# Optimization experiments

Measured on AMD Instinct MI355X. Metric: run time of the kernel, lower is better.

The kernel has to match this reference:

```python
import jax, jax.numpy as jnp
import numpy as np

D_MODEL = 1024
EXPAND = 2
D_INNER = D_MODEL * EXPAND  # 2048
D_STATE = 16
D_CONV = 4
B, T = 4, 2048


def setup_inputs() -> dict:
    key = jax.random.key(0)
    ks = jax.random.split(key, 8)
    s = 0.02  # small init std for numeric stability
    return {
        "x": jax.random.normal(ks[0], (B, T, D_MODEL), jnp.float32),
        "in_proj_w": jax.random.normal(ks[1], (2 * D_INNER, D_MODEL), jnp.float32) * s,
        "conv_w": jax.random.normal(ks[2], (D_INNER, 1, D_CONV), jnp.float32) * s,
        "conv_b": jnp.zeros((D_INNER,), jnp.float32),
        "x_proj_w": jax.random.normal(ks[3], (2 * D_STATE, D_INNER), jnp.float32) * s,
        "dt_proj_w": jax.random.normal(ks[4], (D_INNER, D_STATE), jnp.float32) * s,
        "dt_proj_b": jnp.zeros((D_INNER,), jnp.float32),
        "D_param": jnp.ones((D_INNER,), jnp.float32),
        "out_proj_w": jax.random.normal(ks[5], (D_MODEL, D_INNER), jnp.float32) * s,
    }


def reference(x, in_proj_w, conv_w, conv_b, x_proj_w, dt_proj_w, dt_proj_b, D_param, out_proj_w):
    Bsz, Tlen, _ = x.shape
    # in_proj (no bias), torch Linear: x @ W.T
    xz = jnp.einsum('btd,ed->bte', x, in_proj_w)            # [B,T,2*D_INNER]
    x_inner, z = jnp.split(xz, 2, axis=-1)                   # each [B,T,D_INNER]
    # depthwise causal conv1d: left-pad d_conv-1, take first T outputs
    xc = jnp.transpose(x_inner, (0, 2, 1))                   # [B,D_INNER,T]
    xc = jax.lax.conv_general_dilated(
        xc, conv_w, window_strides=(1,), padding=[(D_CONV - 1, 0)],
        feature_group_count=D_INNER)
    xc = xc + conv_b[None, :, None]
    x_conv = jax.nn.silu(jnp.transpose(xc, (0, 2, 1)))       # [B,T,D_INNER]
    # x_proj -> (B_ssm, C_ssm); C_ssm is unused by the simplified scan (faithful)
    x_ssm = jnp.einsum('btd,ed->bte', x_conv, x_proj_w)      # [B,T,2*D_STATE]
    B_ssm, C_ssm = jnp.split(x_ssm, 2, axis=-1)
    dt = jax.nn.softplus(jnp.einsum('btn,dn->btd', B_ssm, dt_proj_w) + dt_proj_b)  # [B,T,D_INNER]
    # simplified selective scan: EMA with scalar-per-timestep gate
    alpha = jax.nn.sigmoid(jnp.mean(dt, axis=-1, keepdims=True))  # [B,T,1]

    def step(h, inp):
        a, xt = inp
        h = a * h + (1.0 - a) * xt
        return h, h

    aT = jnp.transpose(alpha, (1, 0, 2))   # [T,B,1]
    xT = jnp.transpose(x_conv, (1, 0, 2))  # [T,B,D_INNER]
    h0 = jnp.zeros((Bsz, D_INNER), x.dtype)
    _, ys = jax.lax.scan(step, h0, (aT, xT))
    y = jnp.transpose(ys, (1, 0, 2))        # [B,T,D_INNER]
    y = y * D_param + x_conv                # skip with learned D
    y = y * jax.nn.silu(z)                  # gate
    out = jnp.einsum('btd,ed->bte', y, out_proj_w)  # [B,T,D_MODEL]
    return out
```

## Files before the change

kernel.cpp:

```cpp
#include <hip/hip_runtime.h>
#include <stdint.h>

#define TLEN   2048
#define DMODEL 1024
#define DINNER 2048
#define MROWS  8192
#define NCH    16
#define CHUNK  128

typedef unsigned short u16;
typedef __bf16 bf16x8 __attribute__((ext_vector_type(8)));
typedef float  f32x4  __attribute__((ext_vector_type(4)));

__device__ __forceinline__ float bf2f(u16 u) {
  union { unsigned int i; float f; } v; v.i = ((unsigned int)u) << 16; return v.f;
}
__device__ __forceinline__ u16 f2bf(float f) {
  union { float f; unsigned int u; } v; v.f = f;
  unsigned int u = v.u;
  return (u16)((u + 0x7fffu + ((u >> 16) & 1u)) >> 16);
}
__device__ __forceinline__ float silu_f(float x) { return x / (1.f + __expf(-x)); }

__device__ __forceinline__ void async16(const u16* g, u16* l) {
  __builtin_amdgcn_global_load_lds(
      (const __attribute__((address_space(1))) void*)(g),
      (__attribute__((address_space(3))) void*)(l),
      16, 0, 0);
}

#define BAR      asm volatile("s_barrier" ::: "memory")
#define WAITV(n) asm volatile("s_waitcnt vmcnt(" #n ")" ::: "memory")
#define PRIO1    __builtin_amdgcn_s_setprio(1)
#define PRIO0    __builtin_amdgcn_s_setprio(0)

__global__ __launch_bounds__(256) void k_convert(const float* __restrict__ x,
    const float* __restrict__ w1, const float* __restrict__ w3,
    const float* __restrict__ xpw,
    u16* __restrict__ xb, u16* __restrict__ w1b, u16* __restrict__ w3b,
    u16* __restrict__ xpwb) {
  int i = blockIdx.x * 256 + threadIdx.x;
  const int nx  = MROWS * DMODEL / 4;
  const int nw1 = 2 * DINNER * DMODEL / 4;
  const int nw3 = DMODEL * DINNER / 4;
  const float* src; u16* dst; int j;
  if (i < nx)                  { src = x;   dst = xb;   j = i; }
  else if (i < nx + nw1)       { src = w1;  dst = w1b;  j = i - nx; }
  else if (i < nx + nw1 + nw3) { src = w3;  dst = w3b;  j = i - nx - nw1; }
  else                         { src = xpw; dst = xpwb; j = i - nx - nw1 - nw3; }
  float4 v = ((const float4*)src)[j];
  ushort4 o;
  o.x = f2bf(v.x); o.y = f2bf(v.y); o.z = f2bf(v.z); o.w = f2bf(v.w);
  ((ushort4*)dst)[j] = o;
}

__device__ __forceinline__ u16* regp(u16* lds, int s, int mat, int h) {
  return lds + (((s * 2 + mat) * 2 + h) * 8192);
}

__device__ __forceinline__ void read_a(bf16x8 (&dst)[4][2], const u16* reg,
                                       int qa, int fr, int c0, int c1) {
  #pragma unroll
  for (int m = 0; m < 4; m++) {
    const u16* p = reg + (qa * 64 + m * 16 + fr) * 64;
    dst[m][0] = *(const bf16x8*)(p + c0);
    dst[m][1] = *(const bf16x8*)(p + c1);
  }
}
__device__ __forceinline__ void read_b(bf16x8 (&dst)[2][2], const u16* reg,
                                       int rb, int c0, int c1) {
  #pragma unroll
  for (int n = 0; n < 2; n++) {
    const u16* p = reg + (rb + n * 16) * 64;
    dst[n][0] = *(const bf16x8*)(p + c0);
    dst[n][1] = *(const bf16x8*)(p + c1);
  }
}
__device__ __forceinline__ void mfma_quad(f32x4 (&acc)[8][4],
    const bf16x8 (&af)[4][2], const bf16x8 (&bf)[2][2], int qa, int qb) {
  #pragma unroll
  for (int m = 0; m < 4; m++)
    #pragma unroll
    for (int n = 0; n < 2; n++)
      #pragma unroll
      for (int ks = 0; ks < 2; ks++)
        acc[qa * 4 + m][qb * 2 + n] = __builtin_amdgcn_mfma_f32_16x16x32_bf16(
            af[m][ks], bf[n][ks], acc[qa * 4 + m][qb * 2 + n], 0, 0, 0);
}

template<int N, int K, bool OUT_BF16>
__global__ __launch_bounds__(512) void k_gemm8p(const u16* __restrict__ A,
    const u16* __restrict__ Bm, void* __restrict__ C) {
  static_assert(K % 128 == 0, "K must be multiple of 128");
  extern __shared__ u16 lds[];
  const int tid  = threadIdx.x;
  const int lane = tid & 63;
  const int wave = tid >> 6;
  const int wm   = wave >> 2;
  const int wn   = wave & 3;
  const int fr   = lane & 15;
  const int q    = lane >> 4;

  int wg = blockIdx.x, nwg = gridDim.x, swz = wg;
  if ((nwg & 7) == 0) swz = (wg & 7) * (nwg >> 3) + (wg >> 3);
  const int NT_N = N / 256;
  const size_t blockM = (size_t)(swz / NT_N) * 256;
  const size_t blockN = (size_t)(swz % NT_N) * 256;

  const int rsub   = tid >> 3;
  const int srcCol = 8 * ((tid & 7) ^ (rsub & 7));
  const u16* gA = A  + (blockM + rsub) * (size_t)K + srcCol;
  const u16* gB = Bm + (blockN + rsub) * (size_t)K + srcCol;

#define STAGE(sl, mat, h, kt) do {                                           \
    const u16* _g = ((mat) ? gB : gA) + (size_t)(h) * (128 * (size_t)K)      \
                    + (size_t)(kt) * 64;                                     \
    u16* _l = regp(lds, (sl), (mat), (h)) + tid * 8;                         \
    async16(_g, _l);                                                         \
    async16(_g + (size_t)64 * K, _l + 4096);                                 \
  } while (0)

  const int c0 = (((q * 16)      ^ ((fr & 7) << 4)) >> 1);
  const int c1 = (((64 + q * 16) ^ ((fr & 7) << 4)) >> 1);
  const int rb = (wn & 1) * 64 + fr;

  f32x4 acc[8][4] = {};
  bf16x8 a0[4][2], a1[4][2], bl[2][2], bh[2][2];

  const int NT = K / 64;
  const int NITER = K / 128;

  STAGE(0, 0, 0, 0); STAGE(0, 0, 1, 0); STAGE(0, 1, 0, 0); STAGE(0, 1, 1, 0);
  STAGE(1, 1, 0, 1); STAGE(1, 1, 1, 1); STAGE(1, 0, 0, 1);
  WAITV(6);
  BAR;

  for (int it = 0; it < NITER; ++it) {
    const int t2 = 2 * it + 2, t3 = 2 * it + 3;
    const bool pf = (t2 < NT);
    read_a(a0, regp(lds, 0, 0, wm), 0, fr, c0, c1);
    read_b(bl, regp(lds, 0, 1, wn >> 1), rb, c0, c1);
    STAGE(1, 0, 1, 2 * it + 1);
    BAR;
    PRIO1; mfma_quad(acc, a0, bl, 0, 0); PRIO0;
    BAR;
    read_b(bh, regp(lds, 0, 1, wn >> 1), rb + 32, c0, c1);
    if (pf) STAGE(0, 1, 0, t2);
    BAR;
    PRIO1; mfma_quad(acc, a0, bh, 0, 1); PRIO0;
    BAR;
    read_a(a1, regp(lds, 0, 0, wm), 1, fr, c0, c1);
    if (pf) STAGE(0, 1, 1, t2);
    BAR;
    PRIO1; mfma_quad(acc, a1, bl, 1, 0); PRIO0;
    BAR;
    if (pf) STAGE(0, 0, 0, t2);
    BAR;
    PRIO1; mfma_quad(acc, a1, bh, 1, 1); PRIO0;
    if (pf) { WAITV(6); } else { WAITV(0); }
    BAR;
    read_a(a0, regp(lds, 1, 0, wm), 0, fr, c0, c1);
    read_b(bl, regp(lds, 1, 1, wn >> 1), rb, c0, c1);
    if (pf) STAGE(0, 0, 1, t2);
    BAR;
    PRIO1; mfma_quad(acc, a0, bl, 0, 0); PRIO0;
    BAR;
    read_b(bh, regp(lds, 1, 1, wn >> 1), rb + 32, c0, c1);
    if (pf) STAGE(1, 1, 0, t3);
    BAR;
    PRIO1; mfma_quad(acc, a0, bh, 0, 1); PRIO0;
    BAR;
    read_a(a1, regp(lds, 1, 0, wm), 1, fr, c0, c1);
    if (pf) STAGE(1, 1, 1, t3);
    BAR;
    PRIO1; mfma_quad(acc, a1, bl, 1, 0); PRIO0;
    BAR;
    if (pf) STAGE(1, 0, 0, t3);
    BAR;
    PRIO1; mfma_quad(acc, a1, bh, 1, 1); PRIO0;
    if (pf) { WAITV(6); BAR; } else { BAR; }
  }
#undef STAGE

  {
    const size_t r0  = blockM + (size_t)wm * 128;
    const size_t cc0 = blockN + (size_t)wn * 64;
    #pragma unroll
    for (int m = 0; m < 8; m++)
      #pragma unroll
      for (int n = 0; n < 4; n++)
        #pragma unroll
        for (int r = 0; r < 4; r++) {
          size_t row = r0 + m * 16 + q * 4 + r;
          size_t col = cc0 + n * 16 + fr;
          float v = acc[m][n][r];
          if (OUT_BF16) ((u16*)C)[row * N + col] = f2bf(v);
          else          ((float*)C)[row * N + col] = v;
        }
  }
}

template<int N, int K, bool OUT_BF16>
__global__ __launch_bounds__(256) void k_gemm_bt(const u16* __restrict__ A,
    const u16* __restrict__ B, void* __restrict__ C) {
  __shared__ u16 sA[2][128 * 32];
  __shared__ u16 sB[2][128 * 32];
  const int tid  = threadIdx.x;
  const int lane = tid & 63;
  const int wave = tid >> 6;
  const int wm   = (wave >> 1) * 64;
  const int wn   = (wave & 1) * 64;
  const int fr   = lane & 15;
  const int q    = lane >> 4;
  const size_t blockM = (size_t)blockIdx.y * 128;
  const size_t blockN = (size_t)blockIdx.x * 128;

  const int srow = lane >> 2;
  const int scol = (lane & 3) * 8;
  const u16* gA = A + (blockM + (size_t)wave * 32 + srow) * (size_t)K + scol;
  const u16* gB = B + (blockN + (size_t)wave * 32 + srow) * (size_t)K + scol;
  u16* lA0 = sA[0] + wave * 1024;
  u16* lA1 = sA[1] + wave * 1024;
  u16* lB0 = sB[0] + wave * 1024;
  u16* lB1 = sB[1] + wave * 1024;

  f32x4 acc[4][4] = {};

  for (int kt = 0; kt < K; kt += 64) {
    async16(gA + kt,                        lA0);
    async16(gA + 16 * (size_t)K + kt,       lA0 + 512);
    async16(gA + kt + 32,                   lA1);
    async16(gA + 16 * (size_t)K + kt + 32,  lA1 + 512);
    async16(gB + kt,                        lB0);
    async16(gB + 16 * (size_t)K + kt,       lB0 + 512);
    async16(gB + kt + 32,                   lB1);
    async16(gB + 16 * (size_t)K + kt + 32,  lB1 + 512);
    __syncthreads();

    #pragma unroll
    for (int h = 0; h < 2; h++) {
      bf16x8 af[4], bfr[4];
      #pragma unroll
      for (int tm = 0; tm < 4; tm++)
        af[tm] = *(const bf16x8*)(sA[h] + (wm + tm * 16 + fr) * 32 + q * 8);
      #pragma unroll
      for (int tn = 0; tn < 4; tn++)
        bfr[tn] = *(const bf16x8*)(sB[h] + (wn + tn * 16 + fr) * 32 + q * 8);
      #pragma unroll
      for (int tm = 0; tm < 4; tm++)
        #pragma unroll
        for (int tn = 0; tn < 4; tn++)
          acc[tm][tn] = __builtin_amdgcn_mfma_f32_16x16x32_bf16(
              af[tm], bfr[tn], acc[tm][tn], 0, 0, 0);
    }
    __syncthreads();
  }

  #pragma unroll
  for (int tm = 0; tm < 4; tm++)
    #pragma unroll
    for (int tn = 0; tn < 4; tn++)
      #pragma unroll
      for (int r = 0; r < 4; r++) {
        size_t row = blockM + wm + tm * 16 + q * 4 + r;
        size_t col = blockN + wn + tn * 16 + fr;
        float v = acc[tm][tn][r];
        if (OUT_BF16) ((u16*)C)[row * N + col] = f2bf(v);
        else          ((float*)C)[row * N + col] = v;
      }
}

__global__ __launch_bounds__(256) void k_conv(const u16* __restrict__ xz,
    const float* __restrict__ cw, const float* __restrict__ cb,
    u16* __restrict__ xc) {
  int idx = blockIdx.x * 256 + threadIdx.x;
  int d  = idx & (DINNER - 1);
  int tb = (idx >> 11) & 255;
  int b  = idx >> 19;
  float4 w = ((const float4*)cw)[d];
  float bias = cb[d];
  const u16* inp = xz + ((size_t)(b * TLEN + tb * 8)) * 4096 + d;
  float v[11];
  #pragma unroll
  for (int j = 0; j < 11; j++) {
    int t = tb * 8 - 3 + j;
    v[j] = (t >= 0) ? bf2f(inp[(ptrdiff_t)(j - 3) * 4096]) : 0.f;
  }
  u16* outp = xc + ((size_t)(b * TLEN + tb * 8)) * DINNER + d;
  #pragma unroll
  for (int i = 0; i < 8; i++) {
    float acc = bias + w.x * v[i] + w.y * v[i + 1] + w.z * v[i + 2] + w.w * v[i + 3];
    outp[(size_t)i * DINNER] = f2bf(silu_f(acc));
  }
}

__global__ __launch_bounds__(256) void k_bssm(const u16* __restrict__ xc,
    const u16* __restrict__ xpwb, float* __restrict__ bssm) {
  const int tid  = threadIdx.x;
  const int lane = tid & 63;
  const int wave = tid >> 6;
  const int fr   = lane & 15;
  const int q    = lane >> 4;
  const size_t row0 = (size_t)blockIdx.x * 32;
  const int k0 = wave * 512;

  f32x4 acc[2] = {};
  #pragma unroll
  for (int kk = 0; kk < 512; kk += 32) {
    const int kb = k0 + kk + q * 8;
    bf16x8 bfrag = *(const bf16x8*)(xpwb + (size_t)fr * DINNER + kb);
    #pragma unroll
    for (int tm = 0; tm < 2; tm++) {
      bf16x8 afrag = *(const bf16x8*)(xc + (row0 + tm * 16 + fr) * (size_t)DINNER + kb);
      acc[tm] = __builtin_amdgcn_mfma_f32_16x16x32_bf16(afrag, bfrag, acc[tm], 0, 0, 0);
    }
  }

  __shared__ float red[4][32][16];
  #pragma unroll
  for (int tm = 0; tm < 2; tm++)
    #pragma unroll
    for (int r = 0; r < 4; r++)
      red[wave][tm * 16 + q * 4 + r][fr] = acc[tm][r];
  __syncthreads();
  #pragma unroll
  for (int i = tid; i < 512; i += 256) {
    int r = i >> 4, n = i & 15;
    bssm[(row0 + r) * 16 + n] =
        red[0][r][n] + red[1][r][n] + red[2][r][n] + red[3][r][n];
  }
}

__global__ __launch_bounds__(256) void k_alpha(const float* __restrict__ bssm,
    const float* __restrict__ dtw, const float* __restrict__ dtb,
    float* __restrict__ alpha) {
  const int tid = threadIdx.x;
  const size_t row0 = (size_t)blockIdx.x * 16;
  __shared__ float4 sB[16][4];
  { int r = tid >> 4, n = tid & 15;
    ((float*)&sB[r][0])[n] = bssm[(row0 + r) * 16 + n]; }
  __syncthreads();

  float rowsum[16];
  #pragma unroll
  for (int r = 0; r < 16; r++) rowsum[r] = 0.f;

  #pragma unroll 1
  for (int m = 0; m < 4; m++) {
    const int d0 = m * 512 + tid * 2;
    float4 w[2][4]; float bias[2];
    #pragma unroll
    for (int j = 0; j < 2; j++) {
      const float4* wp = (const float4*)(dtw + (size_t)(d0 + j) * 16);
      w[j][0] = wp[0]; w[j][1] = wp[1]; w[j][2] = wp[2]; w[j][3] = wp[3];
      bias[j] = dtb[d0 + j];
    }
    #pragma unroll
    for (int r = 0; r < 16; r++) {
      float4 b0 = sB[r][0], b1 = sB[r][1], b2 = sB[r][2], b3 = sB[r][3];
      float s = 0.f;
      #pragma unroll
      for (int j = 0; j < 2; j++) {
        float dot = bias[j]
          + b0.x * w[j][0].x + b0.y * w[j][0].y + b0.z * w[j][0].z + b0.w * w[j][0].w
          + b1.x * w[j][1].x + b1.y * w[j][1].y + b1.z * w[j][1].z + b1.w * w[j][1].w
          + b2.x * w[j][2].x + b2.y * w[j][2].y + b2.z * w[j][2].z + b2.w * w[j][2].w
          + b3.x * w[j][3].x + b3.y * w[j][3].y + b3.z * w[j][3].z + b3.w * w[j][3].w;
        s += (dot > 15.f) ? dot : __logf(1.f + __expf(dot));
      }
      rowsum[r] += s;
    }
  }
  #pragma unroll
  for (int r = 0; r < 16; r++)
    #pragma unroll
    for (int off = 32; off > 0; off >>= 1) rowsum[r] += __shfl_xor(rowsum[r], off);
  __shared__ float red[4][16];
  if ((tid & 63) == 0) {
    #pragma unroll
    for (int r = 0; r < 16; r++) red[tid >> 6][r] = rowsum[r];
  }
  __syncthreads();
  if (tid < 16) {
    float mean = (red[0][tid] + red[1][tid] + red[2][tid] + red[3][tid]) * (1.f / DINNER);
    alpha[row0 + tid] = 1.f / (1.f + __expf(-mean));
  }
}

__global__ __launch_bounds__(256) void k_scan1(const u16* __restrict__ xc,
    const float* __restrict__ alpha, float* __restrict__ carry) {
  const int blk = blockIdx.x;
  const int g = blk & 7;
  const int c = (blk >> 3) & 15;
  const int b = blk >> 7;
  const int d = g * 256 + threadIdx.x;
  __shared__ float sa[CHUNK];
  if (threadIdx.x < CHUNK) sa[threadIdx.x] = alpha[b * TLEN + c * CHUNK + threadIdx.x];
  __syncthreads();
  const u16* xp = xc + ((size_t)(b * TLEN + c * CHUNK)) * DINNER + d;
  float h = 0.f;
  #pragma unroll 8
  for (int i = 0; i < CHUNK; i++) {
    float a = sa[i];
    float xv = bf2f(xp[(size_t)i * DINNER]);
    h = a * h + (1.f - a) * xv;
  }
  carry[((size_t)(b * NCH + c)) * DINNER + d] = h;
}

__global__ __launch_bounds__(256) void k_scan2(float* __restrict__ carry,
    const float* __restrict__ alpha) {
  int i = blockIdx.x * 256 + threadIdx.x;
  int b = i >> 11;
  int d = i & (DINNER - 1);
  __shared__ float sP[NCH];
  if (threadIdx.x < NCH) {
    const float* ap = alpha + b * TLEN + threadIdx.x * CHUNK;
    float p = 1.f;
    for (int j = 0; j < CHUNK; j++) p *= ap[j];
    sP[threadIdx.x] = p;
  }
  __syncthreads();
  float h = 0.f;
  #pragma unroll
  for (int c = 0; c < NCH; c++) {
    size_t idx = ((size_t)(b * NCH + c)) * DINNER + d;
    float cv = carry[idx];
    carry[idx] = h;
    h = sP[c] * h + cv;
  }
}

__global__ __launch_bounds__(256) void k_scan3(const u16* __restrict__ xc,
    const u16* __restrict__ xz, const float* __restrict__ alpha,
    const float* __restrict__ Hs, const float* __restrict__ Dp,
    u16* __restrict__ yg) {
  const int blk = blockIdx.x;
  const int g = blk & 7;
  const int c = (blk >> 3) & 15;
  const int b = blk >> 7;
  const int d = g * 256 + threadIdx.x;
  __shared__ float sa[CHUNK];
  if (threadIdx.x < CHUNK) sa[threadIdx.x] = alpha[b * TLEN + c * CHUNK + threadIdx.x];
  __syncthreads();
  float h = Hs[((size_t)(b * NCH + c)) * DINNER + d];
  const float Dv = Dp[d];
  const size_t row0 = (size_t)(b * TLEN + c * CHUNK);
  #pragma unroll 4
  for (int i = 0; i < CHUNK; i++) {
    size_t row = row0 + i;
    float a = sa[i];
    float xv = bf2f(xc[row * DINNER + d]);
    h = a * h + (1.f - a) * xv;
    float zv = bf2f(xz[row * 4096 + DINNER + d]);
    float y = h * Dv + xv;
    yg[row * DINNER + d] = f2bf(y * silu_f(zv));
  }
}

extern "C" void kernel_launch(void* const* d_in, const int* in_sizes, int n_in,
                              void* d_out, int out_size, void* d_ws, size_t ws_size,
                              hipStream_t stream) {
  const float* x   = (const float*)d_in[0];
  const float* w1  = (const float*)d_in[1];
  const float* cw  = (const float*)d_in[2];
  const float* cb  = (const float*)d_in[3];
  const float* xpw = (const float*)d_in[4];
  const float* dtw = (const float*)d_in[5];
  const float* dtb = (const float*)d_in[6];
  const float* Dp  = (const float*)d_in[7];
  const float* w3  = (const float*)d_in[8];
  float* out = (float*)d_out;
  char* ws = (char*)d_ws;

  u16*   xb    = (u16*)(ws + 0);
  u16*   w1b   = (u16*)(ws + 16777216);
  u16*   w3b   = (u16*)(ws + 25165824);
  u16*   xz    = (u16*)(ws + 29360128);
  u16*   xc    = (u16*)(ws + 96468992);
  u16*   yg    = (u16*)(ws + 130023424);
  float* bssm  = (float*)(ws + 163577856);
  float* alpha = (float*)(ws + 164102144);
  float* carry = (float*)(ws + 164135168);
  u16*   xpwb  = (u16*)(ws + 164659456);

  k_convert<<<14368, 256, 0, stream>>>(x, w1, w3, xpw, xb, w1b, w3b, xpwb);
  k_gemm8p<4096, 1024, true><<<512, 512, 131072, stream>>>(xb, w1b, xz);
  k_conv   <<<8192, 256, 0, stream>>>(xz, cw, cb, xc);
  k_bssm   <<<256, 256, 0, stream>>>(xc, xpwb, bssm);
  k_alpha  <<<512, 256, 0, stream>>>(bssm, dtw, dtb, alpha);
  k_scan1  <<<512, 256, 0, stream>>>(xc, alpha, carry);
  k_scan2  <<<32, 256, 0, stream>>>(carry, alpha);
  k_scan3  <<<512, 256, 0, stream>>>(xc, xz, alpha, carry, Dp, yg);
  k_gemm_bt<1024, 2048, false><<<dim3(8, 64), 256, 0, stream>>>(yg, w3b, out);
}
```

Measured before the change: 329.8 us.

## Reschedule GEMM main loop to prefetch LDS fragments one MFMA phase ahead

```diff
diff --git a/kernel.cpp b/kernel.cpp
--- a/kernel.cpp
+++ b/kernel.cpp
@@ -130,55 +130,46 @@
   const int NT = K / 64;
   const int NITER = K / 128;
 
-  STAGE(0, 0, 0, 0); STAGE(0, 0, 1, 0); STAGE(0, 1, 0, 0); STAGE(0, 1, 1, 0);
-  STAGE(1, 1, 0, 1); STAGE(1, 1, 1, 1); STAGE(1, 0, 0, 1);
+  STAGE(0, 1, 0, 0); STAGE(0, 1, 1, 0); STAGE(0, 0, 0, 0); STAGE(0, 0, 1, 0);
+  STAGE(1, 1, 0, 1); STAGE(1, 0, 0, 1); STAGE(1, 0, 1, 1);
   WAITV(6);
   BAR;
+  read_a(a0, regp(lds, 0, 0, wm), 0, fr, c0, c1);
+  read_b(bl, regp(lds, 0, 1, wn >> 1), rb, c0, c1);
 
   for (int it = 0; it < NITER; ++it) {
-    const int t2 = 2 * it + 2, t3 = 2 * it + 3;
+    const int t1 = 2 * it + 1, t2 = 2 * it + 2, t3 = 2 * it + 3;
     const bool pf = (t2 < NT);
-    read_a(a0, regp(lds, 0, 0, wm), 0, fr, c0, c1);
-    read_b(bl, regp(lds, 0, 1, wn >> 1), rb, c0, c1);
-    STAGE(1, 0, 1, 2 * it + 1);
-    BAR;
-    PRIO1; mfma_quad(acc, a0, bl, 0, 0); PRIO0;
-    BAR;
     read_b(bh, regp(lds, 0, 1, wn >> 1), rb + 32, c0, c1);
+    STAGE(1, 1, 1, t1);
+    BAR; PRIO1; mfma_quad(acc, a0, bl, 0, 0); PRIO0; BAR;
+    read_a(a1, regp(lds, 0, 0, wm), 1, fr, c0, c1);
     if (pf) STAGE(0, 1, 0, t2);
-    BAR;
-    PRIO1; mfma_quad(acc, a0, bh, 0, 1); PRIO0;
-    BAR;
-    read_a(a1, regp(lds, 0, 0, wm), 1, fr, c0, c1);
-    if (pf) STAGE(0, 1, 1, t2);
-    BAR;
-    PRIO1; mfma_quad(acc, a1, bl, 1, 0); PRIO0;
-    BAR;
-    if (pf) STAGE(0, 0, 0, t2);
-    BAR;
-    PRIO1; mfma_quad(acc, a1, bh, 1, 1); PRIO0;
-    if (pf) { WAITV(6); } else { WAITV(0); }
+    BAR; PRIO1; mfma_quad(acc, a0, bh, 0, 1); PRIO0;
+    if (pf) { WAITV(4); } else { WAITV(2); }
     BAR;
     read_a(a0, regp(lds, 1, 0, wm), 0, fr, c0, c1);
+    if (pf) STAGE(0, 0, 0, t2);
+    BAR; PRIO1; mfma_quad(acc, a1, bl, 1, 0); PRIO0;
+    if (pf) { WAITV(4); } else { WAITV(0); }
+    BAR;
     read_b(bl, regp(lds, 1, 1, wn >> 1), rb, c0, c1);
     if (pf) STAGE(0, 0, 1, t2);
+    BAR; PRIO1; mfma_quad(acc, a1, bh, 1, 1); PRIO0; BAR;
+    read_b(bh, regp(lds, 1, 1, wn >> 1), rb + 32, c0, c1);
+    if (pf) STAGE(0, 1, 1, t2);
+    BAR; PRIO1; mfma_quad(acc, a0, bl, 0, 0); PRIO0; BAR;
+    read_a(a1, regp(lds, 1, 0, wm), 1, fr, c0, c1);
+    if (pf) STAGE(1, 1, 0, t3);
+    BAR; PRIO1; mfma_quad(acc, a0, bh, 0, 1); PRIO0;
+    WAITV(4);
     BAR;
-    PRIO1; mfma_quad(acc, a0, bl, 0, 0); PRIO0;
+    if (pf) { read_a(a0, regp(lds, 0, 0, wm), 0, fr, c0, c1); STAGE(1, 0, 0, t3); }
+    BAR; PRIO1; mfma_quad(acc, a1, bl, 1, 0); PRIO0;
+    WAITV(4);
     BAR;
-    read_b(bh, regp(lds, 1, 1, wn >> 1), rb + 32, c0, c1);
-    if (pf) STAGE(1, 1, 0, t3);
-    BAR;
-    PRIO1; mfma_quad(acc, a0, bh, 0, 1); PRIO0;
-    BAR;
-    read_a(a1, regp(lds, 1, 0, wm), 1, fr, c0, c1);
-    if (pf) STAGE(1, 1, 1, t3);
-    BAR;
-    PRIO1; mfma_quad(acc, a1, bl, 1, 0); PRIO0;
-    BAR;
-    if (pf) STAGE(1, 0, 0, t3);
-    BAR;
-    PRIO1; mfma_quad(acc, a1, bh, 1, 1); PRIO0;
-    if (pf) { WAITV(6); BAR; } else { BAR; }
+    if (pf) { read_b(bl, regp(lds, 0, 1, wn >> 1), rb, c0, c1); STAGE(1, 0, 1, t3); }
+    BAR; PRIO1; mfma_quad(acc, a1, bh, 1, 1); PRIO0; BAR;
   }
 #undef STAGE
 
```

After: 326.7 us. About the same (-0.9%).
